# Performance work log

Hardware: AMD Instinct MI355X
Metric: run time of the kernel (lower is better)

## Reference

```python
import jax, jax.numpy as jnp
import numpy as np

ITERATIONS = 5


def _dilate3x3(x):
    # 3x3 box 'conv' with all-ones kernel, padding=1 (SAME), single channel, NCHW
    k = jnp.ones((1, 1, 3, 3), x.dtype)
    return jax.lax.conv_general_dilated(
        x, k, window_strides=(1, 1), padding='SAME',
        dimension_numbers=('NCHW', 'OIHW', 'NCHW'))


def setup_inputs() -> dict:
    key = jax.random.key(0)
    k1, k2 = jax.random.split(key)
    H = W = 4096
    prediction = jax.random.uniform(k1, (1, 1, H, W), dtype=jnp.float32)
    ground_truth = jax.random.uniform(k2, (1, 1, H, W), dtype=jnp.float32)
    return {"prediction": prediction, "ground_truth": ground_truth}


def reference(prediction, ground_truth):
    # distance_weight = [1, 4, 9, 16, 25]
    weights = jnp.asarray([(i + 1) ** 2 for i in range(ITERATIONS)], dtype=jnp.float32)
    gt_sum = jnp.sum(ground_truth)
    fn_total = jnp.zeros((), dtype=jnp.float32)
    pred = prediction
    for i in range(ITERATIONS):  # fixed small unrolled loop (sequential recurrence)
        dilated = jnp.clip(_dilate3x3(pred), 0.0, 1.0)
        sharp = jax.nn.sigmoid(20.0 * (dilated - pred - 0.5))
        false_negative = ground_truth * sharp
        fn_total = fn_total + weights[i] * jnp.sum(false_negative) / gt_sum
        pred = pred + false_negative  # fed into next iteration's dilation
    return fn_total
```

## Files before the change

kernel.cpp:

```cpp
#include <hip/hip_runtime.h>

#define N 4096
#define CORE_W 116
#define NSTRIP 36
#define ROWS 18
#define NCHUNK 228
#define ITERS 5
#define NSLOT 32
#define WPB 4
#define NBLOCK ((NSTRIP * NCHUNK) / WPB)


typedef float2 f2;
__device__ __forceinline__ f2 mkf2(float a, float b){ f2 r; r.x=a; r.y=b; return r; }

__device__ __forceinline__ f2 hsum(f2 v) {
    float m = v.x + v.y;
    float L = __shfl_up(v.y, 1);
    float R = __shfl_down(v.x, 1);
    return mkf2(L + m, m + R);
}

__device__ __forceinline__ f2 stepf(f2 p, f2 d, f2 g, f2* fn) {
    const float C1 = 28.853900817779268f;
    const float C2 = 14.426950408889634f;
    f2 o, f;
    {
        float dd = fminf(fmaxf(d.x, 0.f), 1.f);
        float u  = __builtin_fmaf(p.x - dd, C1, C2);
        float sh = __builtin_amdgcn_rcpf(1.f + __builtin_amdgcn_exp2f(u));
        f.x = g.x * sh; o.x = p.x + f.x;
    }
    {
        float dd = fminf(fmaxf(d.y, 0.f), 1.f);
        float u  = __builtin_fmaf(p.y - dd, C1, C2);
        float sh = __builtin_amdgcn_rcpf(1.f + __builtin_amdgcn_exp2f(u));
        f.y = g.y * sh; o.y = p.y + f.y;
    }
    *fn = f;
    return o;
}

__device__ __forceinline__ f2 ldrow(const float* __restrict__ base, int row,
                                    int gc, bool edge) {
    if (row < 0 || row >= N) return mkf2(0.f, 0.f);
    if (!edge) return *(const f2*)(base + (size_t)row * N + gc);
    float a = 0.f, b = 0.f;
    if (gc >= 0 && gc < N)         a = base[(size_t)row * N + gc];
    if (gc + 1 >= 0 && gc + 1 < N) b = base[(size_t)row * N + gc + 1];
    return mkf2(a, b);
}

__global__ __launch_bounds__(64 * WPB, 4) void wlc_main(
    const float* __restrict__ pred,
    const float* __restrict__ gt,
    float* __restrict__ ws)
{
    const int lane   = threadIdx.x & 63;
    const int wid    = threadIdx.x >> 6;
    const int linear = blockIdx.x * WPB + wid;
    const int strip  = linear % NSTRIP;
    const int chunk  = linear / NSTRIP;
    const int x0 = strip * CORE_W - 6;
    const int gc = x0 + 2 * lane;
    const bool edge = (strip == 0) || (strip == NSTRIP - 1);

    const int R0 = chunk * ROWS;
    const int R1 = min(R0 + ROWS, N);
    const int t0 = R0 - 5;
    const int t1 = R1 + 5;

    const float colm = (lane >= 3 && lane <= 60) ? 1.f : 0.f;
    const float m0 = (gc     < N) ? colm : 0.f;
    const float m1 = (gc + 1 < N) ? colm : 0.f;

    f2 pr[6], gb[6];
    f2 h0[3], h1[3], h2[3], h3[3], h4[3];
    f2 o1[2], o2[2], o3[2], o4[2];
#pragma unroll
    for (int i = 0; i < 6; ++i) { pr[i] = mkf2(0,0); gb[i] = mkf2(0,0); }
#pragma unroll
    for (int i = 0; i < 3; ++i) { h0[i]=h1[i]=h2[i]=h3[i]=h4[i]=mkf2(0,0); }
#pragma unroll
    for (int i = 0; i < 2; ++i) { o1[i]=o2[i]=o3[i]=o4[i]=mkf2(0,0); }

    pr[2] = ldrow(pred, t0,     gc, edge);
    pr[3] = ldrow(pred, t0 + 1, gc, edge);

    float s1a=0.f, s2a=0.f, s3a=0.f, s4a=0.f, s5a=0.f, gsa=0.f;

#define S6(o) ((8 + k + (o)) % 6)
#define S3(o) ((8 + k + (o)) % 3)
#define S2(o) ((8 + k + (o)) % 2)

    for (int tb = t0; tb < t1; tb += 6) {
#pragma unroll
        for (int k = 0; k < 6; ++k) {
            const int t = tb + k;
            if (t < t1) {
                const f2 g5 = gb[S6(-5)];
                if (t + 2 <= R1 + 4) pr[S6(2)] = ldrow(pred, t + 2, gc, edge);
                if (t + 1 <= R1 + 3) gb[S6(1)] = ldrow(gt,   t + 1, gc, edge);

                h0[S3(0)] = hsum(pr[S6(0)]);

                f2 d, fn, o;
                d = mkf2(h0[0].x + h0[1].x + h0[2].x, h0[0].y + h0[1].y + h0[2].y);
                o = stepf(pr[S6(-1)], d, gb[S6(-1)], &fn);
                { int r = t - 1; if (r >= R0 && r < R1) s1a += fn.x*m0 + fn.y*m1; }
                h1[S3(-1)] = hsum(o);  o1[S2(-1)] = o;

                d = mkf2(h1[0].x + h1[1].x + h1[2].x, h1[0].y + h1[1].y + h1[2].y);
                o = stepf(o1[S2(-2)], d, gb[S6(-2)], &fn);
                { int r = t - 2; if (r >= R0 && r < R1) s2a += fn.x*m0 + fn.y*m1; }
                h2[S3(-2)] = hsum(o);  o2[S2(-2)] = o;

                d = mkf2(h2[0].x + h2[1].x + h2[2].x, h2[0].y + h2[1].y + h2[2].y);
                o = stepf(o2[S2(-3)], d, gb[S6(-3)], &fn);
                { int r = t - 3; if (r >= R0 && r < R1) s3a += fn.x*m0 + fn.y*m1; }
                h3[S3(-3)] = hsum(o);  o3[S2(-3)] = o;

                d = mkf2(h3[0].x + h3[1].x + h3[2].x, h3[0].y + h3[1].y + h3[2].y);
                o = stepf(o3[S2(-4)], d, gb[S6(-4)], &fn);
                { int r = t - 4; if (r >= R0 && r < R1) s4a += fn.x*m0 + fn.y*m1; }
                h4[S3(-4)] = hsum(o);  o4[S2(-4)] = o;

                d = mkf2(h4[0].x + h4[1].x + h4[2].x, h4[0].y + h4[1].y + h4[2].y);
                o = stepf(o4[S2(-5)], d, g5, &fn);
                { int r = t - 5;
                  if (r >= R0 && r < R1) {
                      s5a += fn.x*m0 + fn.y*m1;
                      gsa += g5.x*m0 + g5.y*m1;
                  } }
            }
        }
    }
#undef S6
#undef S3
#undef S2

    float vals[6] = {gsa, s1a, s2a, s3a, s4a, s5a};
    const int slot = (strip + chunk * NSTRIP) & (NSLOT - 1);
#pragma unroll
    for (int kk = 0; kk < 6; ++kk) {
        float v = vals[kk];
#pragma unroll
        for (int off = 32; off > 0; off >>= 1)
            v += __shfl_down(v, off, 64);
        if (lane == 0) atomicAdd(&ws[slot * 32 + kk], v);
    }
}

__global__ __launch_bounds__(64) void wlc_final(const float* __restrict__ ws,
                                                float* __restrict__ out)
{
    const int lane = threadIdx.x;
    float t[6];
#pragma unroll
    for (int kk = 0; kk < 6; ++kk)
        t[kk] = (lane < NSLOT) ? ws[lane * 32 + kk] : 0.f;
#pragma unroll
    for (int kk = 0; kk < 6; ++kk) {
#pragma unroll
        for (int off = 32; off > 0; off >>= 1)
            t[kk] += __shfl_down(t[kk], off, 64);
    }
    if (lane == 0)
        out[0] = (1.f * t[1] + 4.f * t[2] + 9.f * t[3] + 16.f * t[4] + 25.f * t[5]) / t[0];
}

extern "C" void kernel_launch(void* const* d_in, const int* in_sizes, int n_in,
                              void* d_out, int out_size, void* d_ws, size_t ws_size,
                              hipStream_t stream)
{
    const float* pred = (const float*)d_in[0];
    const float* gtp  = (const float*)d_in[1];
    float* ws = (float*)d_ws;

    hipMemsetAsync(d_ws, 0, NSLOT * 32 * sizeof(float), stream);

    wlc_main<<<dim3(NBLOCK), 64 * WPB, 0, stream>>>(pred, gtp, ws);
    wlc_final<<<1, 64, 0, stream>>>(ws, (float*)d_out);
}
```

Measured before the change: 224.1 us.

## Enlarge row chunks, use running vertical sums, and merge weighted accumulators

Each wave's row chunk grows from 18 to 29 rows, so fewer chunks are needed. This cuts the overhead of recomputing the 5-row halo at chunk edges. The 3-row vertical sum is now carried as a running pair of previous and partial sums, which saves one add per stage. The five per-iteration accumulators are folded into one weighted sum, which shrinks the final reduction to two values and raises the occupancy hint to 5. The risks are longer serial work per wave, fewer waves (less parallelism), and register pressure from the higher occupancy target.

```diff
diff --git a/kernel.cpp b/kernel.cpp
--- a/kernel.cpp
+++ b/kernel.cpp
@@ -3,8 +3,8 @@
 #define N 4096
 #define CORE_W 116
 #define NSTRIP 36
-#define ROWS 18
-#define NCHUNK 228
+#define ROWS 29
+#define NCHUNK 142
 #define ITERS 5
 #define NSLOT 32
 #define WPB 4
@@ -51,7 +51,7 @@
     return mkf2(a, b);
 }
 
-__global__ __launch_bounds__(64 * WPB, 4) void wlc_main(
+__global__ __launch_bounds__(64 * WPB, 5) void wlc_main(
     const float* __restrict__ pred,
     const float* __restrict__ gt,
     float* __restrict__ ws)
@@ -75,22 +75,22 @@
     const float m1 = (gc + 1 < N) ? colm : 0.f;
 
     f2 pr[6], gb[6];
-    f2 h0[3], h1[3], h2[3], h3[3], h4[3];
+    f2 hp0, hp1, hp2, hp3, hp4;
+    f2 ps0, ps1, ps2, ps3, ps4;
     f2 o1[2], o2[2], o3[2], o4[2];
 #pragma unroll
     for (int i = 0; i < 6; ++i) { pr[i] = mkf2(0,0); gb[i] = mkf2(0,0); }
-#pragma unroll
-    for (int i = 0; i < 3; ++i) { h0[i]=h1[i]=h2[i]=h3[i]=h4[i]=mkf2(0,0); }
+    hp0=hp1=hp2=hp3=hp4=mkf2(0,0);
+    ps0=ps1=ps2=ps3=ps4=mkf2(0,0);
 #pragma unroll
     for (int i = 0; i < 2; ++i) { o1[i]=o2[i]=o3[i]=o4[i]=mkf2(0,0); }
 
     pr[2] = ldrow(pred, t0,     gc, edge);
     pr[3] = ldrow(pred, t0 + 1, gc, edge);
 
-    float s1a=0.f, s2a=0.f, s3a=0.f, s4a=0.f, s5a=0.f, gsa=0.f;
+    float sw = 0.f, gsa = 0.f;
 
 #define S6(o) ((8 + k + (o)) % 6)
-#define S3(o) ((8 + k + (o)) % 3)
 #define S2(o) ((8 + k + (o)) % 2)
 
     for (int tb = t0; tb < t1; tb += 6) {
@@ -102,47 +102,61 @@
                 if (t + 2 <= R1 + 4) pr[S6(2)] = ldrow(pred, t + 2, gc, edge);
                 if (t + 1 <= R1 + 3) gb[S6(1)] = ldrow(gt,   t + 1, gc, edge);
 
-                h0[S3(0)] = hsum(pr[S6(0)]);
+                f2 hn, d, fn, o;
 
-                f2 d, fn, o;
-                d = mkf2(h0[0].x + h0[1].x + h0[2].x, h0[0].y + h0[1].y + h0[2].y);
+                hn = hsum(pr[S6(0)]);
+                d  = mkf2(hn.x + ps0.x, hn.y + ps0.y);
+                ps0 = mkf2(hn.x + hp0.x, hn.y + hp0.y);
+                hp0 = hn;
+
                 o = stepf(pr[S6(-1)], d, gb[S6(-1)], &fn);
-                { int r = t - 1; if (r >= R0 && r < R1) s1a += fn.x*m0 + fn.y*m1; }
-                h1[S3(-1)] = hsum(o);  o1[S2(-1)] = o;
+                { int r = t - 1; if (r >= R0 && r < R1)
+                    sw += 1.f * (fn.x*m0 + fn.y*m1); }
+                hn = hsum(o);  o1[S2(-1)] = o;
+                d  = mkf2(hn.x + ps1.x, hn.y + ps1.y);
+                ps1 = mkf2(hn.x + hp1.x, hn.y + hp1.y);
+                hp1 = hn;
 
-                d = mkf2(h1[0].x + h1[1].x + h1[2].x, h1[0].y + h1[1].y + h1[2].y);
                 o = stepf(o1[S2(-2)], d, gb[S6(-2)], &fn);
-                { int r = t - 2; if (r >= R0 && r < R1) s2a += fn.x*m0 + fn.y*m1; }
-                h2[S3(-2)] = hsum(o);  o2[S2(-2)] = o;
+                { int r = t - 2; if (r >= R0 && r < R1)
+                    sw += 4.f * (fn.x*m0 + fn.y*m1); }
+                hn = hsum(o);  o2[S2(-2)] = o;
+                d  = mkf2(hn.x + ps2.x, hn.y + ps2.y);
+                ps2 = mkf2(hn.x + hp2.x, hn.y + hp2.y);
+                hp2 = hn;
 
-                d = mkf2(h2[0].x + h2[1].x + h2[2].x, h2[0].y + h2[1].y + h2[2].y);
                 o = stepf(o2[S2(-3)], d, gb[S6(-3)], &fn);
-                { int r = t - 3; if (r >= R0 && r < R1) s3a += fn.x*m0 + fn.y*m1; }
-                h3[S3(-3)] = hsum(o);  o3[S2(-3)] = o;
+                { int r = t - 3; if (r >= R0 && r < R1)
+                    sw += 9.f * (fn.x*m0 + fn.y*m1); }
+                hn = hsum(o);  o3[S2(-3)] = o;
+                d  = mkf2(hn.x + ps3.x, hn.y + ps3.y);
+                ps3 = mkf2(hn.x + hp3.x, hn.y + hp3.y);
+                hp3 = hn;
 
-                d = mkf2(h3[0].x + h3[1].x + h3[2].x, h3[0].y + h3[1].y + h3[2].y);
                 o = stepf(o3[S2(-4)], d, gb[S6(-4)], &fn);
-                { int r = t - 4; if (r >= R0 && r < R1) s4a += fn.x*m0 + fn.y*m1; }
-                h4[S3(-4)] = hsum(o);  o4[S2(-4)] = o;
+                { int r = t - 4; if (r >= R0 && r < R1)
+                    sw += 16.f * (fn.x*m0 + fn.y*m1); }
+                hn = hsum(o);  o4[S2(-4)] = o;
+                d  = mkf2(hn.x + ps4.x, hn.y + ps4.y);
+                ps4 = mkf2(hn.x + hp4.x, hn.y + hp4.y);
+                hp4 = hn;
 
-                d = mkf2(h4[0].x + h4[1].x + h4[2].x, h4[0].y + h4[1].y + h4[2].y);
                 o = stepf(o4[S2(-5)], d, g5, &fn);
                 { int r = t - 5;
                   if (r >= R0 && r < R1) {
-                      s5a += fn.x*m0 + fn.y*m1;
+                      sw  += 25.f * (fn.x*m0 + fn.y*m1);
                       gsa += g5.x*m0 + g5.y*m1;
                   } }
             }
         }
     }
 #undef S6
-#undef S3
 #undef S2
 
-    float vals[6] = {gsa, s1a, s2a, s3a, s4a, s5a};
+    float vals[2] = {gsa, sw};
     const int slot = (strip + chunk * NSTRIP) & (NSLOT - 1);
 #pragma unroll
-    for (int kk = 0; kk < 6; ++kk) {
+    for (int kk = 0; kk < 2; ++kk) {
         float v = vals[kk];
 #pragma unroll
         for (int off = 32; off > 0; off >>= 1)
@@ -155,18 +169,15 @@
                                                 float* __restrict__ out)
 {
     const int lane = threadIdx.x;
-    float t[6];
+    float t0 = (lane < NSLOT) ? ws[lane * 32 + 0] : 0.f;
+    float t1 = (lane < NSLOT) ? ws[lane * 32 + 1] : 0.f;
 #pragma unroll
-    for (int kk = 0; kk < 6; ++kk)
-        t[kk] = (lane < NSLOT) ? ws[lane * 32 + kk] : 0.f;
-#pragma unroll
-    for (int kk = 0; kk < 6; ++kk) {
-#pragma unroll
-        for (int off = 32; off > 0; off >>= 1)
-            t[kk] += __shfl_down(t[kk], off, 64);
+    for (int off = 32; off > 0; off >>= 1) {
+        t0 += __shfl_down(t0, off, 64);
+        t1 += __shfl_down(t1, off, 64);
     }
     if (lane == 0)
-        out[0] = (1.f * t[1] + 4.f * t[2] + 9.f * t[3] + 16.f * t[4] + 25.f * t[5]) / t[0];
+        out[0] = t1 / t0;
 }
 
 extern "C" void kernel_launch(void* const* d_in, const int* in_sizes, int n_in,
```

After: 232.9 us. 1.04x slower.
